# Kernel tuning notes

Hardware: AMD Instinct MI355X
Metric: run time of the kernel (lower is better)

## Reference

```python
import jax, jax.numpy as jnp
import numpy as np

T, R, I = 16384, 1024, 128   # time steps, reservoir size, input size
CONN, SR = 0.05, 0.9         # connectivity_rate, spectral_radius


def _make_reservoir(rng):
    # Faithful to ESN.create_reservoir_weights: uniform[0,1), sparsify by
    # connectivity_rate, rescale to target spectral radius, flip half the
    # entries' signs.
    W = rng.random((R, R)).astype(np.float32)
    W[rng.random((R, R)) > CONN] = 0.0
    cur_sr = np.max(np.abs(np.linalg.eigvals(W)))
    W = W * (SR / cur_sr)
    neg = rng.choice(R * R, (R * R) // 2, replace=False)
    Wf = W.reshape(-1).copy()
    Wf[neg] *= -1.0
    return Wf.reshape(R, R).astype(np.float32)


def setup_inputs() -> dict:
    rng = np.random.default_rng(0)
    W_res = jnp.asarray(_make_reservoir(rng))
    key = jax.random.key(0)
    k1, k2 = jax.random.split(key)
    X = jax.random.normal(k1, (T, I), dtype=jnp.float32)
    # nn.init.uniform_(w, a=-1, b=1)
    W_in = jax.random.uniform(k2, (R, I), dtype=jnp.float32, minval=-1.0, maxval=1.0)
    state0 = jnp.zeros((R,), dtype=jnp.float32)
    return {"X": X, "W_in": W_in, "W_res": W_res, "state0": state0}


def reference(X, W_in, W_res, state0):
    # state_t = tanh(W_in @ x_t + W_res @ state_{t-1}); collect all states (T, R).
    # Input projections are independent across time -> one big GEMM up front.
    U = X @ W_in.T  # (T, R)

    def step(s, u):
        s = jnp.tanh(u + W_res @ s)
        return s, s

    _, all_states = jax.lax.scan(step, state0, U)
    return all_states  # (T, R), matches update_state's all_states
```

## Files before the change

### kernel.cpp

```cpp
#include <hip/hip_runtime.h>
#include <hip/hip_bf16.h>
#include <stdint.h>


constexpr int T_N = 16384;
constexpr int R_N = 1024;
constexpr int I_N = 128;

constexpr int BT = 64, BR = 64;

__global__ __launch_bounds__(256) void gemm_u_kernel(
    const float* __restrict__ X, const float* __restrict__ Win,
    float* __restrict__ U)
{
    __shared__ float XS[BT][68];
    __shared__ float WS[BR][68];
    const int tid = threadIdx.x;
    const int ty = tid >> 4, tx = tid & 15;
    const int t0 = blockIdx.x * BT;
    const int r0 = blockIdx.y * BR;
    float acc[4][4] = {};

    for (int k0 = 0; k0 < I_N; k0 += 64) {
        for (int idx = tid; idx < BT * 16; idx += 256) {
            int row = idx >> 4, c4 = (idx & 15) << 2;
            *reinterpret_cast<float4*>(&XS[row][c4]) =
                *reinterpret_cast<const float4*>(&X[(size_t)(t0 + row) * I_N + k0 + c4]);
        }
        for (int idx = tid; idx < BR * 16; idx += 256) {
            int row = idx >> 4, c4 = (idx & 15) << 2;
            *reinterpret_cast<float4*>(&WS[row][c4]) =
                *reinterpret_cast<const float4*>(&Win[(size_t)(r0 + row) * I_N + k0 + c4]);
        }
        __syncthreads();
#pragma unroll
        for (int k = 0; k < 64; k += 4) {
            float4 a[4], b[4];
#pragma unroll
            for (int i = 0; i < 4; ++i)
                a[i] = *reinterpret_cast<const float4*>(&XS[ty + 16 * i][k]);
#pragma unroll
            for (int jj = 0; jj < 4; ++jj)
                b[jj] = *reinterpret_cast<const float4*>(&WS[tx + 16 * jj][k]);
#pragma unroll
            for (int i = 0; i < 4; ++i)
#pragma unroll
                for (int jj = 0; jj < 4; ++jj)
                    acc[i][jj] += a[i].x * b[jj].x + a[i].y * b[jj].y +
                                  a[i].z * b[jj].z + a[i].w * b[jj].w;
        }
        __syncthreads();
    }
#pragma unroll
    for (int i = 0; i < 4; ++i)
#pragma unroll
        for (int jj = 0; jj < 4; ++jj)
            U[(size_t)(t0 + ty + 16 * i) * R_N + (r0 + tx + 16 * jj)] = acc[i][jj];
}

constexpr int GBLK    = 8;
constexpr int NLAUNCH = 64;
constexpr int B2      = 1024;
constexpr int RPB     = R_N / GBLK;
constexpr int TPR     = 8;
constexpr int KMAX    = 96;
constexpr int NSL     = KMAX / TPR;
constexpr int FASTCAP = 24;
constexpr int PCAP    = 1 << 20;

__device__ __forceinline__ float fast_tanh(float x) {
    float ax = fabsf(x);
    float e  = __expf(-2.0f * ax);
    float y  = (1.0f - e) / (1.0f + e);
    return copysignf(y, x);
}

__device__ __forceinline__ uint32_t l2_atomic_read(uint32_t* addr) {
    uint32_t old;
    asm volatile("global_atomic_add %0, %1, %2, off sc0\n\t"
                 "s_waitcnt vmcnt(0)"
                 : "=v"(old) : "v"(addr), "v"(0u) : "memory");
    return old;
}

__global__ __launch_bounds__(1024) void esn_scan_kernel(
    const float* __restrict__ Wres, const float* __restrict__ state0,
    float* out, uint32_t* hdr, uint32_t* slots)
{
    __shared__ int   s_role, s_fast;
    __shared__ float sbuf[2][R_N];
    __shared__ uint2 ell[RPB][KMAX];
    __shared__ int   cnt[RPB];

    const int tid = threadIdx.x;

    if (tid == 0) {
        uint32_t xcd;
        asm volatile("s_getreg_b32 %0, hwreg(HW_REG_XCC_ID)" : "=s"(xcd));
        xcd &= 7u;
        uint32_t rank = __hip_atomic_fetch_add(&hdr[xcd], 1u,
                            __ATOMIC_RELAXED, __HIP_MEMORY_SCOPE_AGENT);
        int role = -1;
        if (rank < (uint32_t)GBLK) {
            if (rank == (uint32_t)(GBLK - 1)) {
                uint32_t expected = 0u;
                __hip_atomic_compare_exchange_strong(&hdr[8], &expected, xcd + 1u,
                    __ATOMIC_RELAXED, __ATOMIC_RELAXED, __HIP_MEMORY_SCOPE_AGENT);
            }
            uint32_t win = 0; int sp = 0;
            do {
                win = __hip_atomic_load(&hdr[8], __ATOMIC_RELAXED,
                                        __HIP_MEMORY_SCOPE_AGENT);
            } while (win == 0u && ++sp < PCAP);
            if (win == xcd + 1u) role = (int)rank;
        }
        s_role = role; s_fast = 0;
    }
    __syncthreads();
    const int b = s_role;
    if (b < 0) return;
    const int row0 = b * RPB;

    if (tid == 0) {
        uint32_t* test = hdr + 96;
        if (b == 0) {
            asm volatile("global_store_dword %0, %1, off"
                         :: "v"(test), "v"(0xC0FFEEu) : "memory");
            __hip_atomic_store(&hdr[9], 1u, __ATOMIC_RELAXED,
                               __HIP_MEMORY_SCOPE_AGENT);
        } else {
            int sp = 0;
            while (!__hip_atomic_load(&hdr[9], __ATOMIC_RELAXED,
                                      __HIP_MEMORY_SCOPE_AGENT) && ++sp < PCAP) {}
        }
        uint32_t seen = 0;
        for (int r = 0; r < 32 && !seen; ++r)
            if (l2_atomic_read(test) == 0xC0FFEEu) seen = 1;
        __hip_atomic_store(&hdr[16 + b], seen ? 1u : 2u,
                           __ATOMIC_RELAXED, __HIP_MEMORY_SCOPE_AGENT);
        uint32_t ok = 1;
        for (int i = 0; i < GBLK; ++i) {
            uint32_t v; int sp = 0;
            do { v = __hip_atomic_load(&hdr[16 + i], __ATOMIC_RELAXED,
                                       __HIP_MEMORY_SCOPE_AGENT);
            } while (!v && ++sp < PCAP);
            if (v != 1u) ok = 0;
        }
        s_fast = (int)ok;
    }
    __syncthreads();
    const bool fastp = (s_fast != 0);

    if (tid < RPB) cnt[tid] = 0;
    __syncthreads();
    for (int idx = tid; idx < RPB * R_N; idx += B2) {
        int r = idx >> 10, c = idx & (R_N - 1);
        float w = Wres[(size_t)(row0 + r) * R_N + c];
        if (w != 0.0f) {
            int slot = atomicAdd(&cnt[r], 1);
            if (slot < KMAX) ell[r][slot] = make_uint2((uint32_t)c, __float_as_uint(w));
        }
    }
    __syncthreads();

    const int rloc = tid / TPR;
    const int j    = tid % TPR;
    const int row  = row0 + rloc;
    int   cols[NSL];
    float vals[NSL];
    int   kcnt;
    {
        int myn = cnt[rloc];
        if (myn > KMAX) myn = KMAX;
        kcnt = (myn > j) ? (((myn - 1 - j) >> 3) + 1) : 0;
#pragma unroll
        for (int k = 0; k < NSL; ++k) {
            int slot = j + k * TPR;
            if (slot < myn) {
                uint2 e = ell[rloc][slot];
                cols[k] = (int)e.x;
                vals[k] = __uint_as_float(e.y);
            } else { cols[k] = 0; vals[k] = 0.0f; }
        }
    }

    sbuf[1][tid] = state0[tid];
    float u_cur = (j == 0) ? out[row] : 0.0f;
    __syncthreads();

    for (int t = 0; t < T_N; ++t) {
        const int p = (t - 1) & 1;

        float u_next = 0.0f;
        if (j == 0 && t + 1 < T_N) u_next = out[(size_t)(t + 1) * R_N + row];

        if (t > 0) {
            uint32_t* addr = slots + ((size_t)p << 10) + tid;
            const uint32_t want8 = (uint32_t)(t & 0xFF);
            uint32_t w = 0;
            bool got = false;
            if (fastp) {
                for (int r = 0; r < FASTCAP; ++r) {
                    w = l2_atomic_read(addr);
                    if ((w & 0xFFu) == want8) { got = true; break; }
                }
            }
            if (!got) {
                int sp = 0;
                do {
                    w = __hip_atomic_load(addr, __ATOMIC_RELAXED,
                                          __HIP_MEMORY_SCOPE_AGENT);
                } while ((w & 0xFFu) != want8 && ++sp < PCAP);
            }
            sbuf[p][tid] = __uint_as_float(w & 0xFFFFFF00u);
        }
        __syncthreads();

        float acc = 0.0f;
#pragma unroll
        for (int k = 0; k < NSL; ++k)
            if (k < kcnt) acc += vals[k] * sbuf[p][cols[k]];

        acc += __shfl_xor(acc, 1, TPR);
        acc += __shfl_xor(acc, 2, TPR);
        acc += __shfl_xor(acc, 4, TPR);

        if (j == 0) {
            float y = fast_tanh(u_cur + acc);
            uint32_t bits = __float_as_uint(y);
            uint32_t pkt  = ((bits + 0x80u) & 0xFFFFFF00u)
                          | ((uint32_t)(t + 1) & 0xFFu);
            __hip_atomic_store(&slots[((size_t)(t & 1) << 10) + row], pkt,
                               __ATOMIC_RELAXED, __HIP_MEMORY_SCOPE_AGENT);
            out[(size_t)t * R_N + row] = y;
        }
        u_cur = u_next;
    }
}

extern "C" void kernel_launch(void* const* d_in, const int* in_sizes, int n_in,
                              void* d_out, int out_size, void* d_ws, size_t ws_size,
                              hipStream_t stream)
{
    const float* X      = (const float*)d_in[0];
    const float* W_in   = (const float*)d_in[1];
    const float* W_res  = (const float*)d_in[2];
    const float* state0 = (const float*)d_in[3];
    float* out = (float*)d_out;

    uint32_t* hdr   = (uint32_t*)d_ws;
    uint32_t* slots = (uint32_t*)((char*)d_ws + 1024);

    hipMemsetAsync(d_ws, 0, 1024 + (size_t)2 * R_N * sizeof(uint32_t), stream);

    dim3 g1(T_N / BT, R_N / BR);
    gemm_u_kernel<<<g1, 256, 0, stream>>>(X, W_in, out);

    esn_scan_kernel<<<NLAUNCH, B2, 0, stream>>>(W_res, state0, out, hdr, slots);
}
```

Measured before the change: 24.07 ms.

## Use 64-bit tagged slots, skip own-block polling, sort rows by nnz

```diff
diff --git a/kernel.cpp b/kernel.cpp
--- a/kernel.cpp
+++ b/kernel.cpp
@@ -65,7 +65,6 @@
 constexpr int TPR     = 8;
 constexpr int KMAX    = 96;
 constexpr int NSL     = KMAX / TPR;
-constexpr int FASTCAP = 24;
 constexpr int PCAP    = 1 << 20;
 
 __device__ __forceinline__ float fast_tanh(float x) {
@@ -83,14 +82,24 @@
     return old;
 }
 
+__device__ __forceinline__ unsigned long long l2_load_u64(const void* addr) {
+    unsigned long long v;
+    asm volatile("global_load_dwordx2 %0, %1, off sc0\n\t"
+                 "s_waitcnt vmcnt(0)"
+                 : "=v"(v) : "v"(addr) : "memory");
+    return v;
+}
+
 __global__ __launch_bounds__(1024) void esn_scan_kernel(
     const float* __restrict__ Wres, const float* __restrict__ state0,
-    float* out, uint32_t* hdr, uint32_t* slots)
+    float* out, uint32_t* hdr, unsigned long long* slots)
 {
     __shared__ int   s_role, s_fast;
     __shared__ float sbuf[2][R_N];
     __shared__ uint2 ell[RPB][KMAX];
     __shared__ int   cnt[RPB];
+    __shared__ int   rowmap[RPB];
+    __shared__ int   hist[KMAX + 1];
 
     const int tid = threadIdx.x;
 
@@ -163,16 +172,32 @@
     }
     __syncthreads();
 
-    const int rloc = tid / TPR;
-    const int j    = tid % TPR;
+    if (tid <= KMAX) hist[tid] = 0;
+    __syncthreads();
+    if (tid < RPB) atomicAdd(&hist[min(cnt[tid], KMAX)], 1);
+    __syncthreads();
+    if (tid == 0) {
+        int run = 0;
+        for (int i = 0; i <= KMAX; ++i) { int c = hist[i]; hist[i] = run; run += c; }
+    }
+    __syncthreads();
+    if (tid < RPB) {
+        int c = min(cnt[tid], KMAX);
+        int pos = atomicAdd(&hist[c], 1);
+        rowmap[pos] = tid;
+    }
+    __syncthreads();
+
+    const int rloc = rowmap[tid >> 3];
+    const int j    = tid & 7;
     const int row  = row0 + rloc;
     int   cols[NSL];
     float vals[NSL];
-    int   kcnt;
+    int   kw;
     {
         int myn = cnt[rloc];
         if (myn > KMAX) myn = KMAX;
-        kcnt = (myn > j) ? (((myn - 1 - j) >> 3) + 1) : 0;
+        int kcnt = (myn > j) ? (((myn - 1 - j) >> 3) + 1) : 0;
 #pragma unroll
         for (int k = 0; k < NSL; ++k) {
             int slot = j + k * TPR;
@@ -182,6 +207,13 @@
                 vals[k] = __uint_as_float(e.y);
             } else { cols[k] = 0; vals[k] = 0.0f; }
         }
+        kw = kcnt;
+#pragma unroll
+        for (int off = 1; off < 64; off <<= 1) {
+            int o = __shfl_xor(kw, off, 64);
+            kw = (o > kw) ? o : kw;
+        }
+        kw = __builtin_amdgcn_readfirstlane(kw);
     }
 
     sbuf[1][tid] = state0[tid];
@@ -194,32 +226,42 @@
         float u_next = 0.0f;
         if (j == 0 && t + 1 < T_N) u_next = out[(size_t)(t + 1) * R_N + row];
 
-        if (t > 0) {
-            uint32_t* addr = slots + ((size_t)p << 10) + tid;
-            const uint32_t want8 = (uint32_t)(t & 0xFF);
-            uint32_t w = 0;
+        if (t > 0 && (tid >> 7) != b) {
+            unsigned long long* slot = slots + ((size_t)p << 10) + tid;
+            const uint32_t want = (uint32_t)t;
+            unsigned long long w = 0;
             bool got = false;
             if (fastp) {
-                for (int r = 0; r < FASTCAP; ++r) {
-                    w = l2_atomic_read(addr);
-                    if ((w & 0xFFu) == want8) { got = true; break; }
+                w = l2_load_u64(slot);
+                got = ((uint32_t)(w >> 32) == want);
+                int sp = 0;
+                while (!got && ++sp < PCAP) {
+                    uint32_t tg = l2_atomic_read((uint32_t*)slot + 1);
+                    if (tg == want) {
+                        w = ((unsigned long long)tg << 32) |
+                            (unsigned long long)l2_atomic_read((uint32_t*)slot);
+                        got = true;
+                    }
                 }
             }
             if (!got) {
                 int sp = 0;
                 do {
-                    w = __hip_atomic_load(addr, __ATOMIC_RELAXED,
+                    w = __hip_atomic_load(slot, __ATOMIC_RELAXED,
                                           __HIP_MEMORY_SCOPE_AGENT);
-                } while ((w & 0xFFu) != want8 && ++sp < PCAP);
+                } while ((uint32_t)(w >> 32) != want && ++sp < PCAP);
             }
-            sbuf[p][tid] = __uint_as_float(w & 0xFFFFFF00u);
+            sbuf[p][tid] = __uint_as_float((uint32_t)w);
         }
         __syncthreads();
 
+        const float* sb = sbuf[p];
         float acc = 0.0f;
 #pragma unroll
-        for (int k = 0; k < NSL; ++k)
-            if (k < kcnt) acc += vals[k] * sbuf[p][cols[k]];
+        for (int k = 0; k < NSL; ++k) {
+            if (k >= kw) break;
+            acc = fmaf(vals[k], sb[cols[k]], acc);
+        }
 
         acc += __shfl_xor(acc, 1, TPR);
         acc += __shfl_xor(acc, 2, TPR);
@@ -227,12 +269,16 @@
 
         if (j == 0) {
             float y = fast_tanh(u_cur + acc);
-            uint32_t bits = __float_as_uint(y);
-            uint32_t pkt  = ((bits + 0x80u) & 0xFFFFFF00u)
-                          | ((uint32_t)(t + 1) & 0xFFu);
-            __hip_atomic_store(&slots[((size_t)(t & 1) << 10) + row], pkt,
-                               __ATOMIC_RELAXED, __HIP_MEMORY_SCOPE_AGENT);
             out[(size_t)t * R_N + row] = y;
+            sbuf[t & 1][row] = y;
+            unsigned long long w = ((unsigned long long)(uint32_t)(t + 1) << 32)
+                                 | (unsigned long long)__float_as_uint(y);
+            unsigned long long* slot = slots + ((size_t)(t & 1) << 10) + row;
+            if (fastp)
+                *(volatile unsigned long long*)slot = w;
+            else
+                __hip_atomic_store(slot, w, __ATOMIC_RELAXED,
+                                   __HIP_MEMORY_SCOPE_AGENT);
         }
         u_cur = u_next;
     }
@@ -248,10 +294,12 @@
     const float* state0 = (const float*)d_in[3];
     float* out = (float*)d_out;
 
-    uint32_t* hdr   = (uint32_t*)d_ws;
-    uint32_t* slots = (uint32_t*)((char*)d_ws + 1024);
-
-    hipMemsetAsync(d_ws, 0, 1024 + (size_t)2 * R_N * sizeof(uint32_t), stream);
+    uint32_t* hdr = (uint32_t*)d_ws;
+    unsigned long long* slots =
+        (unsigned long long*)((char*)d_ws + 1024);
+
+    hipMemsetAsync(d_ws, 0, 1024 + (size_t)2 * R_N * sizeof(unsigned long long),
+                   stream);
 
     dim3 g1(T_N / BT, R_N / BR);
     gemm_u_kernel<<<g1, 256, 0, stream>>>(X, W_in, out);
```

After: 41.25 ms. +71.3%, slower.
